# Kernel optimization log

Hardware: AMD Instinct MI355X
Metric: run time of the kernel (lower is better)

## Reference

```python
import math
import jax, jax.numpy as jnp
import numpy as np

# ---- module hyperparameters (from init_kwargs) ----
IN_DIM = 3
OUT_DIM = 128
K = 16
SIGMA = 0.3        # base_sigma for both GPE variants
BASELINE = 0.1
SCALING = 10.0
EPS = 1e-6

FEAT_DIM = math.ceil(OUT_DIM / IN_DIM)          # 43
FEAT_NUM = FEAT_DIM * IN_DIM                    # 129
# torch.linspace(0, feat_num-1, out_dim).long() truncates toward zero
OUT_IDX = np.linspace(0.0, FEAT_NUM - 1, OUT_DIM).astype(np.int32)
# torch.linspace(-1,1,feat_dim+2)[1:-1]
FEAT_VAL = np.linspace(-1.0, 1.0, FEAT_DIM + 2)[1:-1].astype(np.float32)


def setup_inputs() -> dict:
    key = jax.random.key(0)
    xyz = jax.random.normal(key, (8, 4096, 3), dtype=jnp.float32)
    return {"xyz": xyz}


def _knn(xyz, k):
    """cdist + topk kNN (excluding self), gather neighbor coords. xyz: [B,N,3] -> [B,N,K,3]."""
    sq = jnp.sum(xyz * xyz, axis=-1)                              # [B,N]
    d2 = sq[:, :, None] + sq[:, None, :] - 2.0 * jnp.einsum('bnd,bmd->bnm', xyz, xyz)
    # squared distance has same ordering as torch.cdist; topk smallest = topk(-d2)
    _, idx = jax.lax.top_k(-d2, k + 1)                            # [B,N,K+1]
    idx = idx[:, :, 1:]                                           # drop self
    neigh = jax.vmap(lambda pts, ix: pts[ix])(xyz, idx)           # [B,N,K,3]
    return neigh


def _blend_weights(neigh):
    """PCA/eigh curvature -> sigmoid blend weights. neigh: [B,N,K,3] -> [B,N,1]."""
    centered = neigh - jnp.mean(neigh, axis=2, keepdims=True)
    cov = jnp.einsum('bnki,bnkj->bnij', centered, centered) / (K - 1)   # [B,N,3,3]
    eig = jnp.linalg.eigvalsh(cov)                                      # ascending, [B,N,3]
    curv = eig[..., 0] / (jnp.sum(eig, axis=-1) + 1e-6)                 # [B,N]
    curv = curv[..., None]                                              # [B,N,1]
    return jax.nn.sigmoid(10.0 * (curv - jnp.mean(curv, axis=1, keepdims=True)))


def _gpe1(xyz):
    """AdaptiveEmbeddingGPE_1: global-std adaptive sigma, Gaussian-cosine blend."""
    gstd = jnp.mean(jnp.std(xyz, axis=1, ddof=1))                 # torch.std is unbiased
    asig = SIGMA * (1.0 + gstd)
    blend = jax.nn.sigmoid((gstd - BASELINE) * SCALING)
    fv = jnp.asarray(FEAT_VAL)                                    # [F]
    tmp = xyz[..., :, None] - fv                                  # [B,N,3,F]
    t = tmp / (asig + EPS)
    comb = blend * jnp.exp(-0.5 * t * t) + (1.0 - blend) * jnp.cos(t)
    comb = comb.reshape(xyz.shape[0], xyz.shape[1], IN_DIM * FEAT_DIM)  # concat over in_dim
    return comb[..., jnp.asarray(OUT_IDX)]                        # [B,N,out_dim]


def _gpe2(xyz, neigh):
    """AdaptiveEmbeddingGPE_2 ('variance'): per-point local-std adaptive RBF."""
    lstd = jnp.std(neigh - xyz[:, :, None, :], axis=2, ddof=1)    # [B,N,3]
    asig = SIGMA * (1.0 + lstd)
    fv = jnp.asarray(FEAT_VAL)
    tmp = xyz[..., :, None] - fv                                  # [B,N,3,F]
    t = tmp / (asig[..., None] + EPS)
    rbf = jnp.exp(-0.5 * t * t)
    rbf = rbf.reshape(xyz.shape[0], xyz.shape[1], IN_DIM * FEAT_DIM)
    return rbf[..., jnp.asarray(OUT_IDX)]                         # [B,N,out_dim]


def reference(xyz):
    neigh = _knn(xyz, K)                  # [B,N,K,3] cdist+topk+gather
    w = _blend_weights(neigh)             # [B,N,1]  eigh curvature blend
    e1 = _gpe1(xyz)                       # [B,N,out_dim]
    e2 = _gpe2(xyz, neigh)                # [B,N,out_dim]
    return w * e1 + (1.0 - w) * e2        # [B,N,out_dim]
```

## Files before the change

kernel.cpp:

```cpp
#include <hip/hip_runtime.h>
#include <math.h>


#define NPTS 4096
#define KNN 17
#define BLKT 512
#define QPB 64
#define ESIZE 512
#define SEG 256
#define SCAP 17

#define WS_CURV  0
#define WS_RAS2  32768
#define WS_CSUM  131072
#define WS_STAT  131584

typedef unsigned long long ull;
#define SENT 0xFFFFFFFFFFFFFFFFULL

__device__ __forceinline__ float d2p(float4 c, float qx, float qy, float qz) {
    return __builtin_fmaf(c.x, qx, __builtin_fmaf(c.y, qy,
           __builtin_fmaf(c.z, qz, c.w)));
}

__device__ __forceinline__ unsigned encf(float f) {
    unsigned u = __float_as_uint(f);
    return u ^ (unsigned)(((int)u >> 31) | 0x80000000u);
}

__device__ __forceinline__ void insertp(ull v, bool ins, ull (&md)[KNN],
                                        ull& maxv, int& maxp) {
#pragma unroll
    for (int k = 0; k < KNN; k++) {
        bool sel = ins && (k == maxp);
        md[k] = sel ? v : md[k];
    }
    maxv = md[0]; maxp = 0;
#pragma unroll
    for (int k = 1; k < KNN; k++) {
        bool g = md[k] > maxv;
        maxv = g ? md[k] : maxv;
        maxp = g ? k : maxp;
    }
}

__device__ __forceinline__ float curv_from_cov(float c00, float c01, float c02,
                                               float c11, float c12, float c22) {
    double a00 = c00, a01 = c01, a02 = c02, a11 = c11, a12 = c12, a22 = c22;
    double tr = a00 + a11 + a22;
    double q  = tr * (1.0 / 3.0);
    double b00 = a00 - q, b11 = a11 - q, b22 = a22 - q;
    double p2 = b00 * b00 + b11 * b11 + b22 * b22
              + 2.0 * (a01 * a01 + a02 * a02 + a12 * a12);
    double lmin;
    if (p2 < 1e-60) {
        lmin = q;
    } else {
        double p  = sqrt(p2 * (1.0 / 6.0));
        double ip = 1.0 / p;
        double m00 = b00 * ip, m11 = b11 * ip, m22 = b22 * ip;
        double m01 = a01 * ip, m02 = a02 * ip, m12 = a12 * ip;
        double det = m00 * (m11 * m22 - m12 * m12)
                   - m01 * (m01 * m22 - m12 * m02)
                   + m02 * (m01 * m12 - m11 * m02);
        double r = 0.5 * det;
        r = r > 1.0 ? 1.0 : (r < -1.0 ? -1.0 : r);
        double phi = acos(r) * (1.0 / 3.0);
        lmin = q + 2.0 * p * cos(phi + 2.0943951023931953);
    }
    return (float)(lmin / (tr + 1e-6));
}

__global__ __launch_bounds__(BLKT, 4) void knn_kernel(const float* __restrict__ xyz,
                                                      float* __restrict__ ws) {
    __shared__ float4 pts[NPTS];
    __shared__ ull aux[1088];
    unsigned char* sbuf = (unsigned char*)aux;
    unsigned short* pub = (unsigned short*)aux;
    int b = blockIdx.x >> 6;
    int chunk = blockIdx.x & 63;
    int tid = threadIdx.x;
    const float* base = xyz + b * NPTS * 3;
    for (int p = tid; p < NPTS; p += BLKT) {
        float x = base[p * 3], y = base[p * 3 + 1], z = base[p * 3 + 2];
        float w = __builtin_fmaf(z, z, __builtin_fmaf(y, y, x * x));
        pts[p] = make_float4(-2.0f * x, -2.0f * y, -2.0f * z, w);
    }
    __syncthreads();

    if (chunk == 0) {
        double sx = 0, sy = 0, sz = 0, qxx = 0, qyy = 0, qzz = 0;
        for (int p = tid; p < NPTS; p += BLKT) {
            float4 c = pts[p];
            float x = -0.5f * c.x, y = -0.5f * c.y, z = -0.5f * c.z;
            sx += (double)x; sy += (double)y; sz += (double)z;
            qxx += (double)x * x; qyy += (double)y * y; qzz += (double)z * z;
        }
        for (int off = 32; off > 0; off >>= 1) {
            sx += __shfl_down(sx, off);  sy += __shfl_down(sy, off);
            sz += __shfl_down(sz, off);  qxx += __shfl_down(qxx, off);
            qyy += __shfl_down(qyy, off); qzz += __shfl_down(qzz, off);
        }
        double* dstat = (double*)aux;
        int wid = tid >> 6;
        if ((tid & 63) == 0) {
            dstat[wid * 6 + 0] = sx;  dstat[wid * 6 + 1] = sy;  dstat[wid * 6 + 2] = sz;
            dstat[wid * 6 + 3] = qxx; dstat[wid * 6 + 4] = qyy; dstat[wid * 6 + 5] = qzz;
        }
        __syncthreads();
        if (tid == 0) {
            double* wd = (double*)(ws + WS_STAT);
            for (int qq = 0; qq < 6; qq++) {
                double a = 0.0;
                for (int w = 0; w < 8; w++) a += dstat[w * 6 + qq];
                wd[b * 6 + qq] = a;
            }
        }
        __syncthreads();
    }

    int wv = tid >> 6;
    int lane = tid & 63;
    int i = chunk * QPB + lane;
    float4 qc = pts[i];
    float qx = -0.5f * qc.x, qy = -0.5f * qc.y, qz = -0.5f * qc.z;
    int cbase = wv * ESIZE;

    float md[KNN];
#pragma unroll
    for (int k = 0; k < KNN; k++) md[k] = 3.4e38f;

#define LADDER(c) { \
    float d2 = d2p((c), qx, qy, qz); \
    _Pragma("unroll") \
    for (int k = KNN - 1; k >= 1; k--) \
        md[k] = __builtin_amdgcn_fmed3f(d2, md[k - 1], md[k]); \
    md[0] = fminf(d2, md[0]); }

    {
        float4 A[8], B[8];
#pragma unroll
        for (int u = 0; u < 8; u++) A[u] = pts[cbase + u];
        for (int m = 0; m < ESIZE - 16; m += 16) {
#pragma unroll
            for (int u = 0; u < 8; u++) B[u] = pts[cbase + m + 8 + u];
#pragma unroll
            for (int u = 0; u < 8; u++) LADDER(A[u]);
#pragma unroll
            for (int u = 0; u < 8; u++) A[u] = pts[cbase + m + 16 + u];
#pragma unroll
            for (int u = 0; u < 8; u++) LADDER(B[u]);
        }
#pragma unroll
        for (int u = 0; u < 8; u++) B[u] = pts[cbase + ESIZE - 8 + u];
#pragma unroll
        for (int u = 0; u < 8; u++) LADDER(A[u]);
#pragma unroll
        for (int u = 0; u < 8; u++) LADDER(B[u]);
    }
#undef LADDER
    float tau = md[KNN - 1];

    ull k17[KNN];
#pragma unroll
    for (int k = 0; k < KNN; k++) k17[k] = SENT;
    ull maxv = SENT; int maxp = 0;

#define P2BODY(c, off) { \
    float d2 = d2p((c), qx, qy, qz); \
    if (d2 <= tau) {                     \
        if (cnt < SCAP) sbuf[cnt * BLKT + tid] = (unsigned char)(off); \
        cnt++; } }

#pragma unroll
    for (int sgi = 0; sgi < 2; sgi++) {
        int segbase = cbase + sgi * SEG;
        int cnt = 0;
        {
            float4 A[4], B[4];
#pragma unroll
            for (int u = 0; u < 4; u++) A[u] = pts[segbase + u];
            for (int m = 0; m < SEG - 8; m += 8) {
#pragma unroll
                for (int u = 0; u < 4; u++) B[u] = pts[segbase + m + 4 + u];
#pragma unroll
                for (int u = 0; u < 4; u++) P2BODY(A[u], m + u);
#pragma unroll
                for (int u = 0; u < 4; u++) A[u] = pts[segbase + m + 8 + u];
#pragma unroll
                for (int u = 0; u < 4; u++) P2BODY(B[u], m + 4 + u);
            }
#pragma unroll
            for (int u = 0; u < 4; u++) B[u] = pts[segbase + SEG - 4 + u];
#pragma unroll
            for (int u = 0; u < 4; u++) P2BODY(A[u], SEG - 8 + u);
#pragma unroll
            for (int u = 0; u < 4; u++) P2BODY(B[u], SEG - 4 + u);
        }
#pragma unroll
        for (int t = 0; t < SCAP; t++) {
            if (__any(t < cnt)) {
                int ix = segbase + sbuf[t * BLKT + tid];
                float4 c = pts[ix];
                float d2 = d2p(c, qx, qy, qz);
                ull key = ((ull)encf(d2) << 32) | (unsigned)ix;
                bool ins = (t < cnt) && (key < maxv);
                if (__any(ins)) insertp(key, ins, k17, maxv, maxp);
            }
        }
    }
#undef P2BODY

    __syncthreads();
    if (wv & 1) {
#pragma unroll
        for (int k = 0; k < KNN; k++)
            pub[(wv >> 1) * 1088 + lane * KNN + k] = (unsigned short)(k17[k] & 0xffffULL);
    }
    __syncthreads();
    if (!(wv & 1)) {
        int r = wv >> 1;
#pragma unroll
        for (int k = 0; k < KNN; k++) {
            int ix = pub[r * 1088 + lane * KNN + k];
            float4 c = pts[ix];
            float d2 = d2p(c, qx, qy, qz);
            ull key = ((ull)encf(d2) << 32) | (unsigned)ix;
            bool ins = key < maxv;
            if (__any(ins)) insertp(key, ins, k17, maxv, maxp);
        }
    }
    __syncthreads();
    if (wv == 2 || wv == 6) {
#pragma unroll
        for (int k = 0; k < KNN; k++)
            pub[(wv >> 2) * 1088 + lane * KNN + k] = (unsigned short)(k17[k] & 0xffffULL);
    }
    __syncthreads();
    if (wv == 0 || wv == 4) {
        int r = wv >> 2;
#pragma unroll
        for (int k = 0; k < KNN; k++) {
            int ix = pub[r * 1088 + lane * KNN + k];
            float4 c = pts[ix];
            float d2 = d2p(c, qx, qy, qz);
            ull key = ((ull)encf(d2) << 32) | (unsigned)ix;
            bool ins = key < maxv;
            if (__any(ins)) insertp(key, ins, k17, maxv, maxp);
        }
    }
    __syncthreads();
    if (wv == 4) {
#pragma unroll
        for (int k = 0; k < KNN; k++)
            pub[lane * KNN + k] = (unsigned short)(k17[k] & 0xffffULL);
    }
    __syncthreads();

    if (wv == 0) {
#pragma unroll
        for (int k = 0; k < KNN; k++) {
            int ix = pub[lane * KNN + k];
            float4 c = pts[ix];
            float d2 = d2p(c, qx, qy, qz);
            ull key = ((ull)encf(d2) << 32) | (unsigned)ix;
            bool ins = key < maxv;
            if (__any(ins)) insertp(key, ins, k17, maxv, maxp);
        }

        float s1x = 0, s1y = 0, s1z = 0;
        float cxx = 0, cxy = 0, cxz = 0, cyy = 0, cyz = 0, czz = 0;
#pragma unroll
        for (int k = 0; k < KNN; k++) {
            int j = (int)(k17[k] & 0xffffffffULL);
            float4 c = pts[j];
            float ux = -0.5f * c.x - qx;
            float uy = -0.5f * c.y - qy;
            float uz = -0.5f * c.z - qz;
            s1x += ux; s1y += uy; s1z += uz;
            cxx += ux * ux; cxy += ux * uy; cxz += ux * uz;
            cyy += uy * uy; cyz += uy * uz; czz += uz * uz;
        }
        const float i16 = 1.0f / 16.0f, i15 = 1.0f / 15.0f;
        float mx = s1x * i16, my = s1y * i16, mz = s1z * i16;
        float c00 = (cxx - 16.0f * mx * mx) * i15;
        float c01 = (cxy - 16.0f * mx * my) * i15;
        float c02 = (cxz - 16.0f * mx * mz) * i15;
        float c11 = (cyy - 16.0f * my * my) * i15;
        float c12 = (cyz - 16.0f * my * mz) * i15;
        float c22 = (czz - 16.0f * mz * mz) * i15;

        float curv = curv_from_cov(c00, c01, c02, c11, c12, c22);

        float v0 = c00 > 0.0f ? c00 : 0.0f;
        float v1 = c11 > 0.0f ? c11 : 0.0f;
        float v2 = c22 > 0.0f ? c22 : 0.0f;
        float r2x = 1.0f / (0.3f * (1.0f + sqrtf(v0)) + 1e-6f);
        float r2y = 1.0f / (0.3f * (1.0f + sqrtf(v1)) + 1e-6f);
        float r2z = 1.0f / (0.3f * (1.0f + sqrtf(v2)) + 1e-6f);

        int g = b * NPTS + i;
        ws[WS_CURV + g] = curv;
        ws[WS_RAS2 + 0 * 32768 + g] = r2x;
        ws[WS_RAS2 + 1 * 32768 + g] = r2y;
        ws[WS_RAS2 + 2 * 32768 + g] = r2z;

        float cs = curv;
        for (int off = 32; off > 0; off >>= 1) cs += __shfl_down(cs, off);
        if (lane == 0) ws[WS_CSUM + b * 64 + chunk] = cs;
    }
}

__global__ void out_kernel(const float* __restrict__ xyz,
                           const float* __restrict__ ws,
                           float* __restrict__ out) {
    __shared__ float sc[3];
    __shared__ float scm[8];
    if (threadIdx.x < 64) {
        float part = 0.0f;
        if (threadIdx.x < 24) {
            const double* st = (const double*)(ws + WS_STAT);
            int bb = threadIdx.x / 3, dd = threadIdx.x % 3;
            double s = st[bb * 6 + dd], ss = st[bb * 6 + 3 + dd];
            double var = (ss - s * s / 4096.0) / 4095.0;
            part = (float)sqrt(var > 0.0 ? var : 0.0);
        }
        float p2 = part;
        for (int off = 32; off > 0; off >>= 1) p2 += __shfl_down(p2, off);
        if (threadIdx.x == 0) {
            float gf = p2 * (1.0f / 24.0f);
            float denom = 0.3f * (1.0f + gf) + 1e-6f;
            float blend = 1.0f / (1.0f + __expf(-(gf - 0.1f) * 10.0f));
            sc[0] = 1.0f / denom;
            sc[1] = blend;
            sc[2] = 1.0f - blend;
        }
        float cp = 0.0f;
        const float* pf = ws + WS_CSUM;
#pragma unroll
        for (int t = 0; t < 8; t++) cp += pf[threadIdx.x * 8 + t];
        cp += __shfl_down(cp, 4);
        cp += __shfl_down(cp, 2);
        cp += __shfl_down(cp, 1);
        if ((threadIdx.x & 7) == 0) scm[threadIdx.x >> 3] = cp * (1.0f / 4096.0f);
    }
    __syncthreads();

    int q4 = blockIdx.x * 256 + (int)threadIdx.x;
    int j0 = (q4 & 31) << 2;
    int g  = q4 >> 5;
    int b  = g >> 12;
    float rasig1 = sc[0];
    float blend  = sc[1];
    float blendc = sc[2];
    float curv   = ws[WS_CURV + g];
    float w = 1.0f / (1.0f + __expf(-10.0f * (curv - scm[b])));
    float wc = 1.0f - w;

    float o[4];
#pragma unroll
    for (int e = 0; e < 4; e++) {
        int j = j0 + e;
        int f = (j < 127) ? j : 128;
        int d = (f >= 86) ? 2 : ((f >= 43) ? 1 : 0);
        int t = f - d * 43;
        float fv = (float)((double)(t + 1) * (2.0 / 44.0) - 1.0);
        float x = xyz[g * 3 + d];
        float t1 = (x - fv) * rasig1;
        float e1 = blend * __expf(-0.5f * t1 * t1) + blendc * __cosf(t1);
        float t2 = (x - fv) * ws[WS_RAS2 + (d << 15) + g];
        float e2 = __expf(-0.5f * t2 * t2);
        o[e] = w * e1 + wc * e2;
    }
    *(float4*)(out + ((long)q4 << 2)) = make_float4(o[0], o[1], o[2], o[3]);
}

extern "C" void kernel_launch(void* const* d_in, const int* in_sizes, int n_in,
                              void* d_out, int out_size, void* d_ws, size_t ws_size,
                              hipStream_t stream) {
    const float* xyz = (const float*)d_in[0];
    float* out = (float*)d_out;
    float* ws = (float*)d_ws;

    knn_kernel<<<512, BLKT, 0, stream>>>(xyz, ws);
    out_kernel<<<out_size / 1024, 256, 0, stream>>>(xyz, ws, out);
}
```

Baseline: 244.8 us.

## Fuse kNN and output kernels via atomic grid barrier

Merges the kNN/curvature kernel and the output embedding kernel into one launch. Per-point curvature and local inverse sigmas stay in shared memory instead of a global round trip, and the reductions move to global atomics. A spin-wait grid barrier then gives every block the global mean curvature and std. This removes one launch and the workspace traffic, but it needs all 512 blocks to be co-resident and adds a memset plus atomic spinning.

```diff
diff --git a/kernel.cpp b/kernel.cpp
--- a/kernel.cpp
+++ b/kernel.cpp
@@ -9,11 +9,10 @@
 #define ESIZE 512
 #define SEG 256
 #define SCAP 17
-
-#define WS_CURV  0
-#define WS_RAS2  32768
-#define WS_CSUM  131072
-#define WS_STAT  131584
+#define NBLK 512
+
+#define WS_CSA 1
+#define WS_GSA 9
 
 typedef unsigned long long ull;
 #define SENT 0xFFFFFFFFFFFFFFFFULL
@@ -71,12 +70,18 @@
     return (float)(lmin / (tr + 1e-6));
 }
 
-__global__ __launch_bounds__(BLKT, 4) void knn_kernel(const float* __restrict__ xyz,
-                                                      float* __restrict__ ws) {
+__global__ __launch_bounds__(BLKT, 4) void fused_kernel(const float* __restrict__ xyz,
+                                                        float* __restrict__ ws,
+                                                        float* __restrict__ out) {
     __shared__ float4 pts[NPTS];
     __shared__ ull aux[1088];
+    __shared__ double dstat[48];
+    __shared__ float sc[4];
+    __shared__ float curv_l[QPB];
+    __shared__ float r2l[3][QPB];
     unsigned char* sbuf = (unsigned char*)aux;
     unsigned short* pub = (unsigned short*)aux;
+
     int b = blockIdx.x >> 6;
     int chunk = blockIdx.x & 63;
     int tid = threadIdx.x;
@@ -101,7 +106,6 @@
             sz += __shfl_down(sz, off);  qxx += __shfl_down(qxx, off);
             qyy += __shfl_down(qyy, off); qzz += __shfl_down(qzz, off);
         }
-        double* dstat = (double*)aux;
         int wid = tid >> 6;
         if ((tid & 63) == 0) {
             dstat[wid * 6 + 0] = sx;  dstat[wid * 6 + 1] = sy;  dstat[wid * 6 + 2] = sz;
@@ -109,14 +113,19 @@
         }
         __syncthreads();
         if (tid == 0) {
-            double* wd = (double*)(ws + WS_STAT);
+            double S[6];
             for (int qq = 0; qq < 6; qq++) {
                 double a = 0.0;
                 for (int w = 0; w < 8; w++) a += dstat[w * 6 + qq];
-                wd[b * 6 + qq] = a;
+                S[qq] = a;
             }
-        }
-        __syncthreads();
+            double stds = 0.0;
+            for (int dd = 0; dd < 3; dd++) {
+                double var = (S[3 + dd] - S[dd] * S[dd] / 4096.0) / 4095.0;
+                stds += sqrt(var > 0.0 ? var : 0.0);
+            }
+            atomicAdd(&ws[WS_GSA], (float)stds);
+        }
     }
 
     int wv = tid >> 6;
@@ -295,84 +304,69 @@
         float v0 = c00 > 0.0f ? c00 : 0.0f;
         float v1 = c11 > 0.0f ? c11 : 0.0f;
         float v2 = c22 > 0.0f ? c22 : 0.0f;
-        float r2x = 1.0f / (0.3f * (1.0f + sqrtf(v0)) + 1e-6f);
-        float r2y = 1.0f / (0.3f * (1.0f + sqrtf(v1)) + 1e-6f);
-        float r2z = 1.0f / (0.3f * (1.0f + sqrtf(v2)) + 1e-6f);
-
-        int g = b * NPTS + i;
-        ws[WS_CURV + g] = curv;
-        ws[WS_RAS2 + 0 * 32768 + g] = r2x;
-        ws[WS_RAS2 + 1 * 32768 + g] = r2y;
-        ws[WS_RAS2 + 2 * 32768 + g] = r2z;
+
+        curv_l[lane] = curv;
+        r2l[0][lane] = 1.0f / (0.3f * (1.0f + sqrtf(v0)) + 1e-6f);
+        r2l[1][lane] = 1.0f / (0.3f * (1.0f + sqrtf(v1)) + 1e-6f);
+        r2l[2][lane] = 1.0f / (0.3f * (1.0f + sqrtf(v2)) + 1e-6f);
 
         float cs = curv;
         for (int off = 32; off > 0; off >>= 1) cs += __shfl_down(cs, off);
-        if (lane == 0) ws[WS_CSUM + b * 64 + chunk] = cs;
-    }
-}
-
-__global__ void out_kernel(const float* __restrict__ xyz,
-                           const float* __restrict__ ws,
-                           float* __restrict__ out) {
-    __shared__ float sc[3];
-    __shared__ float scm[8];
-    if (threadIdx.x < 64) {
-        float part = 0.0f;
-        if (threadIdx.x < 24) {
-            const double* st = (const double*)(ws + WS_STAT);
-            int bb = threadIdx.x / 3, dd = threadIdx.x % 3;
-            double s = st[bb * 6 + dd], ss = st[bb * 6 + 3 + dd];
-            double var = (ss - s * s / 4096.0) / 4095.0;
-            part = (float)sqrt(var > 0.0 ? var : 0.0);
-        }
-        float p2 = part;
-        for (int off = 32; off > 0; off >>= 1) p2 += __shfl_down(p2, off);
-        if (threadIdx.x == 0) {
-            float gf = p2 * (1.0f / 24.0f);
-            float denom = 0.3f * (1.0f + gf) + 1e-6f;
-            float blend = 1.0f / (1.0f + __expf(-(gf - 0.1f) * 10.0f));
-            sc[0] = 1.0f / denom;
-            sc[1] = blend;
-            sc[2] = 1.0f - blend;
-        }
-        float cp = 0.0f;
-        const float* pf = ws + WS_CSUM;
-#pragma unroll
-        for (int t = 0; t < 8; t++) cp += pf[threadIdx.x * 8 + t];
-        cp += __shfl_down(cp, 4);
-        cp += __shfl_down(cp, 2);
-        cp += __shfl_down(cp, 1);
-        if ((threadIdx.x & 7) == 0) scm[threadIdx.x >> 3] = cp * (1.0f / 4096.0f);
-    }
-    __syncthreads();
-
-    int q4 = blockIdx.x * 256 + (int)threadIdx.x;
-    int j0 = (q4 & 31) << 2;
-    int g  = q4 >> 5;
-    int b  = g >> 12;
-    float rasig1 = sc[0];
-    float blend  = sc[1];
-    float blendc = sc[2];
-    float curv   = ws[WS_CURV + g];
-    float w = 1.0f / (1.0f + __expf(-10.0f * (curv - scm[b])));
-    float wc = 1.0f - w;
-
-    float o[4];
-#pragma unroll
-    for (int e = 0; e < 4; e++) {
-        int j = j0 + e;
-        int f = (j < 127) ? j : 128;
-        int d = (f >= 86) ? 2 : ((f >= 43) ? 1 : 0);
-        int t = f - d * 43;
-        float fv = (float)((double)(t + 1) * (2.0 / 44.0) - 1.0);
-        float x = xyz[g * 3 + d];
-        float t1 = (x - fv) * rasig1;
-        float e1 = blend * __expf(-0.5f * t1 * t1) + blendc * __cosf(t1);
-        float t2 = (x - fv) * ws[WS_RAS2 + (d << 15) + g];
-        float e2 = __expf(-0.5f * t2 * t2);
-        o[e] = w * e1 + wc * e2;
-    }
-    *(float4*)(out + ((long)q4 << 2)) = make_float4(o[0], o[1], o[2], o[3]);
+        if (lane == 0) atomicAdd(&ws[WS_CSA + b], cs);
+    }
+
+    __syncthreads();
+    if (tid == 0) {
+        __threadfence();
+        unsigned* ctr = (unsigned*)ws;
+        atomicAdd(ctr, 1u);
+        while (atomicAdd(ctr, 0u) < (unsigned)NBLK)
+            __builtin_amdgcn_s_sleep(32);
+        __threadfence();
+        float cmean = atomicAdd(&ws[WS_CSA + b], 0.0f) * (1.0f / 4096.0f);
+        float gf    = atomicAdd(&ws[WS_GSA], 0.0f) * (1.0f / 24.0f);
+        float denom = 0.3f * (1.0f + gf) + 1e-6f;
+        float blend = 1.0f / (1.0f + __expf(-(gf - 0.1f) * 10.0f));
+        sc[0] = 1.0f / denom;
+        sc[1] = blend;
+        sc[2] = 1.0f - blend;
+        sc[3] = cmean;
+    }
+    __syncthreads();
+
+    {
+        int q  = tid >> 3;
+        int j0 = (tid & 7) << 4;
+        float4 qp = pts[chunk * QPB + q];
+        float xq0 = -0.5f * qp.x, xq1 = -0.5f * qp.y, xq2 = -0.5f * qp.z;
+        float r20 = r2l[0][q], r21 = r2l[1][q], r22 = r2l[2][q];
+        float curv = curv_l[q];
+        float w  = 1.0f / (1.0f + __expf(-10.0f * (curv - sc[3])));
+        float wc = 1.0f - w;
+        float rasig1 = sc[0], blend = sc[1], blendc = sc[2];
+
+        float o[16];
+#pragma unroll
+        for (int e = 0; e < 16; e++) {
+            int j = j0 + e;
+            int f = (j < 127) ? j : 128;
+            int d = (f >= 86) ? 2 : ((f >= 43) ? 1 : 0);
+            int t = f - d * 43;
+            float fv = (float)((double)(t + 1) * (2.0 / 44.0) - 1.0);
+            float x  = (d == 0) ? xq0 : ((d == 1) ? xq1 : xq2);
+            float r2 = (d == 0) ? r20 : ((d == 1) ? r21 : r22);
+            float t1 = (x - fv) * rasig1;
+            float e1 = blend * __expf(-0.5f * t1 * t1) + blendc * __cosf(t1);
+            float t2 = (x - fv) * r2;
+            float e2 = __expf(-0.5f * t2 * t2);
+            o[e] = w * e1 + wc * e2;
+        }
+        float* op = out + ((long)(b * NPTS + chunk * QPB + q) << 7) + j0;
+#pragma unroll
+        for (int v = 0; v < 4; v++)
+            *(float4*)(op + v * 4) = make_float4(o[v * 4], o[v * 4 + 1],
+                                                 o[v * 4 + 2], o[v * 4 + 3]);
+    }
 }
 
 extern "C" void kernel_launch(void* const* d_in, const int* in_sizes, int n_in,
@@ -382,6 +376,6 @@
     float* out = (float*)d_out;
     float* ws = (float*)d_ws;
 
-    knn_kernel<<<512, BLKT, 0, stream>>>(xyz, ws);
-    out_kernel<<<out_size / 1024, 256, 0, stream>>>(xyz, ws, out);
-}
+    hipMemsetAsync(d_ws, 0, 64, stream);
+    fused_kernel<<<NBLK, BLKT, 0, stream>>>(xyz, ws, out);
+}
```

New measurement: 283.5 us. 15.8% more time.
